# Performance work log

Hardware: AMD Instinct MI355X
Metric: run time of the kernel (lower is better)

## Reference

```python
import jax, jax.numpy as jnp
import numpy as np

D_MODEL = 64
HEADS = 8
LEVELS = 5
POINTS = 4
DH = D_MODEL // HEADS
EPS = 1e-5


def _layernorm(x, g, b):
    m = x.mean(-1, keepdims=True)
    v = ((x - m) ** 2).mean(-1, keepdims=True)
    return (x - m) / jnp.sqrt(v + EPS) * g + b


def _bilinear_sample(v, lx, ly, Hl, Wl):
    # v: (B, heads, Hl, Wl, dh); lx, ly: (B, Nq, heads, P) normalized in ~[0,1]
    # matches F.grid_sample(align_corners=False, padding_mode='zeros')
    x = lx * Wl - 0.5
    y = ly * Hl - 0.5
    x0 = jnp.floor(x)
    y0 = jnp.floor(y)
    wx = x - x0
    wy = y - y0
    x0i = x0.astype(jnp.int32)
    y0i = y0.astype(jnp.int32)
    B, heads = v.shape[0], v.shape[1]
    bidx = jnp.arange(B)[:, None, None, None]
    hidx = jnp.arange(heads)[None, None, :, None]

    def gather(yi, xi):
        valid = (xi >= 0) & (xi < Wl) & (yi >= 0) & (yi < Hl)
        xc = jnp.clip(xi, 0, Wl - 1)
        yc = jnp.clip(yi, 0, Hl - 1)
        g = v[bidx, hidx, yc, xc]  # (B, Nq, heads, P, dh)
        return g * valid[..., None].astype(v.dtype)

    return (gather(y0i, x0i) * ((1 - wx) * (1 - wy))[..., None]
            + gather(y0i, x0i + 1) * (wx * (1 - wy))[..., None]
            + gather(y0i + 1, x0i) * ((1 - wx) * wy)[..., None]
            + gather(y0i + 1, x0i + 1) * (wx * wy)[..., None])


def setup_inputs() -> dict:
    key = jax.random.key(0)
    ks = jax.random.split(key, 24)
    B, NQ = 2, 20000
    ss = np.array([[184, 184], [92, 92], [46, 46], [23, 23], [12, 12]], dtype=np.int64)
    areas = ss[:, 0] * ss[:, 1]
    lsi = np.concatenate([[0], np.cumsum(areas)[:-1]]).astype(np.int64)
    LIN = int(areas.sum())  # 45109
    s = 0.02
    inp = {
        'q_feat': jax.random.normal(ks[0], (B, NQ, D_MODEL), jnp.float32),
        'dense_voxel_flatten': jax.random.normal(ks[1], (B, LIN, D_MODEL), jnp.float32),
        'reference_points': jax.random.uniform(ks[2], (B, NQ, 2), jnp.float32),
        'q_pos': jax.random.normal(ks[3], (B, NQ, D_MODEL), jnp.float32),
        'spatial_shapes': ss,
        'level_start_index': lsi,
        'Wv': jax.random.normal(ks[4], (D_MODEL, D_MODEL), jnp.float32) * s,
        'bv': jnp.zeros((D_MODEL,), jnp.float32),
        'Wo': jax.random.normal(ks[5], (D_MODEL, HEADS * LEVELS * POINTS * 2), jnp.float32) * s,
        'bo': jax.random.normal(ks[6], (HEADS * LEVELS * POINTS * 2,), jnp.float32),
        'Wa': jax.random.normal(ks[7], (D_MODEL, HEADS * LEVELS * POINTS), jnp.float32) * s,
        'ba': jnp.zeros((HEADS * LEVELS * POINTS,), jnp.float32),
        'Wout': jax.random.normal(ks[8], (D_MODEL, D_MODEL), jnp.float32) * s,
        'bout': jnp.zeros((D_MODEL,), jnp.float32),
        'g1': jnp.ones((D_MODEL,), jnp.float32),
        'b1': jnp.zeros((D_MODEL,), jnp.float32),
        'W1': jax.random.normal(ks[9], (D_MODEL, 1024), jnp.float32) * s,
        'bff1': jnp.zeros((1024,), jnp.float32),
        'W2': jax.random.normal(ks[10], (1024, D_MODEL), jnp.float32) * s,
        'bff2': jnp.zeros((D_MODEL,), jnp.float32),
        'g2': jnp.ones((D_MODEL,), jnp.float32),
        'b2': jnp.zeros((D_MODEL,), jnp.float32),
    }
    return inp


def reference(q_feat, dense_voxel_flatten, reference_points, q_pos,
              spatial_shapes, level_start_index,
              Wv, bv, Wo, bo, Wa, ba, Wout, bout,
              g1, b1, W1, bff1, W2, bff2, g2, b2):
    B, NQ, _ = q_feat.shape
    q = q_feat + q_pos  # with_pos_embed
    value = (dense_voxel_flatten @ Wv + bv).reshape(B, -1, HEADS, DH)
    off = (q @ Wo + bo).reshape(B, NQ, HEADS, LEVELS, POINTS, 2)
    aw = jax.nn.softmax((q @ Wa + ba).reshape(B, NQ, HEADS, LEVELS * POINTS), axis=-1)
    aw = aw.reshape(B, NQ, HEADS, LEVELS, POINTS)
    # offset normalizer is (W, H) per level
    ssn = np.asarray(spatial_shapes)
    normalizer = jnp.asarray(ssn[:, ::-1].copy(), q.dtype)  # (L, 2)
    loc = reference_points[:, :, None, None, None, :] + off / normalizer[None, None, None, :, None, :]
    out = jnp.zeros((B, NQ, HEADS, DH), q.dtype)
    for l in range(LEVELS):
        Hl, Wl = int(ssn[l, 0]), int(ssn[l, 1])
        st = int(np.asarray(level_start_index)[l])
        vl = value[:, st:st + Hl * Wl].reshape(B, Hl, Wl, HEADS, DH).transpose(0, 3, 1, 2, 4)
        sampled = _bilinear_sample(vl, loc[:, :, :, l, :, 0], loc[:, :, :, l, :, 1], Hl, Wl)
        out = out + jnp.einsum('bnhpd,bnhp->bnhd', sampled, aw[:, :, :, l])
    attn_out = out.reshape(B, NQ, D_MODEL) @ Wout + bout
    x = _layernorm(q_feat + attn_out, g1, b1)  # residual + norm1 (dropout=0)
    ffn = jax.nn.relu(x @ W1 + bff1) @ W2 + bff2
    return _layernorm(x + ffn, g2, b2)
```

## Files before the change

kernel.cpp:

```cpp
#include <hip/hip_runtime.h>
#include <hip/hip_bf16.h>

#define NB 2
#define NQ 20000
#define DM 64
#define NH 8
#define NL 5
#define NP 4
#define LIN 45109
#define FFN 1024

typedef __attribute__((ext_vector_type(8))) short short8;
typedef __attribute__((ext_vector_type(4))) float f32x4;

__device__ __forceinline__ float b2f(const __hip_bfloat16 h) { return __bfloat162float(h); }
__device__ __forceinline__ float lo16f(unsigned u) { return __uint_as_float(u << 16); }
__device__ __forceinline__ float hi16f(unsigned u) { return __uint_as_float(u & 0xffff0000u); }
__device__ __forceinline__ unsigned f2bf_bits(float x) {
    unsigned u = __float_as_uint(x);
    return (u + 0x7FFFu + ((u >> 16) & 1u)) >> 16;
}

__global__ void __launch_bounds__(256)
val_proj_kernel(const float* __restrict__ dvf,
                const float* __restrict__ Wv,
                const float* __restrict__ bv,
                __hip_bfloat16* __restrict__ valA,
                __hip_bfloat16* __restrict__ valB,
                int rows) {
    __shared__ __align__(16) __hip_bfloat16 wvp[8][64][8];
    __shared__ __align__(16) __hip_bfloat16 ar[64][72];
    __shared__ __align__(16) float bvs[64];

    const int tid = threadIdx.x;
    const int lane = tid & 63;
    const int w = tid >> 6;
    const int m16 = lane & 15, qd = lane >> 4;
    const int row0 = blockIdx.x * 64;

    for (int idx = tid; idx < 4096; idx += 256) {
        const int j = idx & 7;
        const int l = (idx >> 3) & 63;
        const int seg = idx >> 9;
        const int nt = seg >> 1, kc = seg & 1;
        const int n = nt * 16 + (l & 15);
        const int k = kc * 32 + (l >> 4) * 8 + j;
        wvp[seg][l][j] = __float2bfloat16(Wv[k * 64 + n]);
    }
    if (tid < 64) bvs[tid] = bv[tid];

    {
        const int r = w * 16 + m16;
        const int grow = row0 + r;
        const int c0 = qd * 16;
        __hip_bfloat16* dst = &ar[r][c0];
        if (grow < rows) {
            const float4* src = (const float4*)&dvf[(size_t)grow * DM + c0];
#pragma unroll
            for (int t = 0; t < 4; t++) {
                const float4 v = src[t];
                dst[t * 4 + 0] = __float2bfloat16(v.x);
                dst[t * 4 + 1] = __float2bfloat16(v.y);
                dst[t * 4 + 2] = __float2bfloat16(v.z);
                dst[t * 4 + 3] = __float2bfloat16(v.w);
            }
        } else {
#pragma unroll
            for (int t = 0; t < 16; t++) dst[t] = __float2bfloat16(0.f);
        }
    }
    __syncthreads();

    f32x4 acc[4];
#pragma unroll
    for (int nt = 0; nt < 4; nt++) acc[nt] = (f32x4){0.f, 0.f, 0.f, 0.f};
#pragma unroll
    for (int kc = 0; kc < 2; kc++) {
        const short8 a = *(const short8*)&ar[w * 16 + m16][kc * 32 + qd * 8];
#pragma unroll
        for (int nt = 0; nt < 4; nt++) {
            const short8 b = *(const short8*)&wvp[nt * 2 + kc][lane][0];
            acc[nt] = __builtin_amdgcn_mfma_f32_16x16x32_bf16(a, b, acc[nt], 0, 0, 0);
        }
    }

#pragma unroll
    for (int r = 0; r < 4; r++) {
        const int gr = row0 + w * 16 + qd * 4 + r;
        if (gr < rows) {
            const int vr = (gr < LIN) ? gr : gr - LIN;
            __hip_bfloat16* dst = (gr < LIN) ? valA : valB;
#pragma unroll
            for (int nt = 0; nt < 4; nt++) {
                const int c = nt * 16 + m16;
                dst[((size_t)(c >> 3) * LIN + vr) * 8 + (c & 7)] =
                    __float2bfloat16(acc[nt][r] + bvs[c]);
            }
        }
    }
}

__global__ void pack_kernel(const float* __restrict__ W1, const float* __restrict__ W2,
                            const float* __restrict__ Wo, const float* __restrict__ Wa,
                            const float* __restrict__ Wout,
                            __hip_bfloat16* __restrict__ W1p, __hip_bfloat16* __restrict__ W2p,
                            __hip_bfloat16* __restrict__ Woap, __hip_bfloat16* __restrict__ Woutp) {
    const int t = blockIdx.x * 256 + threadIdx.x;
    const int lane = t & 63;
    const int m = lane & 15, qd = lane >> 4;
    const int seg = t >> 6;
    if (seg < 128) {
        const int nt = seg >> 1, kc = seg & 1;
        const int n = nt * 16 + m, kb = kc * 32 + qd * 8;
        __hip_bfloat16* dst = W1p + ((size_t)seg * 64 + lane) * 8;
#pragma unroll
        for (int j = 0; j < 8; j++) dst[j] = __float2bfloat16(W1[(size_t)(kb + j) * FFN + n]);
    } else if (seg < 256) {
        const int sl = seg - 128;
        const int nt = sl >> 5, kc = sl & 31;
        const int n = nt * 16 + m, kb = kc * 32 + qd * 8;
        __hip_bfloat16* dst = W2p + ((size_t)sl * 64 + lane) * 8;
#pragma unroll
        for (int j = 0; j < 8; j++) dst[j] = __float2bfloat16(W2[(size_t)(kb + j) * DM + n]);
    } else if (seg < 316) {
        const int sl = seg - 256;
        const int nt = sl >> 1, kc = sl & 1;
        const int n = nt * 16 + m, kb = kc * 32 + qd * 8;
        __hip_bfloat16* dst = Woap + ((size_t)sl * 64 + lane) * 8;
#pragma unroll
        for (int j = 0; j < 8; j++) {
            const int k = kb + j;
            const float v = (n < 320) ? Wo[(size_t)k * 320 + n] : Wa[(size_t)k * 160 + (n - 320)];
            dst[j] = __float2bfloat16(v);
        }
    } else if (seg < 324) {
        const int sl = seg - 316;
        const int nt = sl >> 1, kc = sl & 1;
        const int n = nt * 16 + m, kb = kc * 32 + qd * 8;
        __hip_bfloat16* dst = Woutp + ((size_t)sl * 64 + lane) * 8;
#pragma unroll
        for (int j = 0; j < 8; j++) dst[j] = __float2bfloat16(Wout[(size_t)(kb + j) * DM + n]);
    }
}

__global__ void __launch_bounds__(256, 8)
attn4_kernel(const float* __restrict__ q_feat,
             const float* __restrict__ ref_pts,
             const float* __restrict__ q_pos,
             const __hip_bfloat16* __restrict__ Woap,
             const float* __restrict__ bo, const float* __restrict__ ba,
             const __hip_bfloat16* __restrict__ Woutp, const float* __restrict__ bout,
             const float* __restrict__ g1, const float* __restrict__ b1,
             const __hip_bfloat16* __restrict__ valA,
             const __hip_bfloat16* __restrict__ valB,
             int qoff,
             float* __restrict__ xout) {
    __shared__ __align__(16) __hip_bfloat16 qb[16][72];
    __shared__ __align__(16) float offs[4][321];
    __shared__ __align__(16) float aws[4][161];
    __shared__ __align__(16) float refs[4][2];
    __shared__ __align__(16) int4  dsc[640];

    float (*xs4)[64] = (float(*)[64])offs;

    const int tid = threadIdx.x;
    const int lane = tid & 63;
    const int w = tid >> 6;
    const int m16 = lane & 15, qd = lane >> 4;
    const int q0 = qoff + blockIdx.x * 4;
    const int qi = q0 + w;

    const int sz[NL]  = {184, 92, 46, 23, 12};
    const int lsi[NL] = {0, 33856, 42320, 44436, 44965};

    const __hip_bfloat16* valp = (q0 >= NQ) ? valB : valA;

    const float qf = q_feat[(size_t)qi * DM + lane];
    const float qp = q_pos[(size_t)qi * DM + lane];
    qb[w][lane] = __float2bfloat16(qf + qp);
    for (int idx = tid; idx < 12 * 64; idx += 256)
        qb[4 + (idx >> 6)][idx & 63] = __float2bfloat16(0.f);
    if (tid < 8) refs[tid >> 1][tid & 1] = ref_pts[(size_t)(q0 + (tid >> 1)) * 2 + (tid & 1)];
    __syncthreads();

    for (int nt = w; nt < 30; nt += 4) {
        f32x4 acc = {0.f, 0.f, 0.f, 0.f};
#pragma unroll
        for (int kc = 0; kc < 2; kc++) {
            const short8 a = *(const short8*)&qb[m16][kc * 32 + qd * 8];
            const short8 b = *(const short8*)(Woap + ((size_t)(nt * 2 + kc) * 64 + lane) * 8);
            acc = __builtin_amdgcn_mfma_f32_16x16x32_bf16(a, b, acc, 0, 0, 0);
        }
        if (qd == 0) {
            const int n = nt * 16 + m16;
            if (n < 320) {
                const float bn = bo[n];
#pragma unroll
                for (int r = 0; r < 4; r++) offs[r][n] = acc[r] + bn;
            } else {
                const float bn = ba[n - 320];
#pragma unroll
                for (int r = 0; r < 4; r++) aws[r][n - 320] = acc[r] + bn;
            }
        }
    }
    __syncthreads();

    {
        const int g = tid >> 3;
        const int q = g >> 3, h = g & 7;
        const int j = tid & 7;
        float* p = &aws[q][h * 20];
        const float v0 = p[j], v1 = p[j + 8];
        const float v2 = (j < 4) ? p[j + 16] : -1e30f;
        float mx = fmaxf(fmaxf(v0, v1), v2);
        mx = fmaxf(mx, __shfl_xor(mx, 1, 8));
        mx = fmaxf(mx, __shfl_xor(mx, 2, 8));
        mx = fmaxf(mx, __shfl_xor(mx, 4, 8));
        const float e0 = __expf(v0 - mx), e1 = __expf(v1 - mx);
        const float e2 = (j < 4) ? __expf(v2 - mx) : 0.f;
        float s = e0 + e1 + e2;
        s += __shfl_xor(s, 1, 8);
        s += __shfl_xor(s, 2, 8);
        s += __shfl_xor(s, 4, 8);
        const float inv = 1.f / s;
        p[j] = e0 * inv;
        p[j + 8] = e1 * inv;
        if (j < 4) p[j + 16] = e2 * inv;
    }
    __syncthreads();

    for (int s = tid; s < 640; s += 256) {
        const int h = s & 7;
        const int t2 = s >> 3;
        const int p = t2 & 3;
        const int t3 = t2 >> 2;
        const int l = t3 % 5;
        const int q = t3 / 5;
        const int Wl = sz[l];
        const float Wf = (float)Wl;
        const int st = lsi[l];
        const int c = ((h * 5 + l) * 4 + p) * 2;
        const float fx = fmaf(refs[q][0], Wf, offs[q][c]) - 0.5f;
        const float fy = fmaf(refs[q][1], Wf, offs[q][c + 1]) - 0.5f;
        const float x0f = floorf(fx), y0f = floorf(fy);
        const float wx = fx - x0f, wy = fy - y0f;
        const int x0 = (int)x0f, y0 = (int)y0f;
        const float aV = aws[q][h * 20 + l * 4 + p];
        const bool xin0 = (x0 >= 0) & (x0 < Wl);
        const bool xin1 = (x0 >= -1) & (x0 < Wl - 1);
        const bool yin0 = (y0 >= 0) & (y0 < Wl);
        const bool yin1 = (y0 >= -1) & (y0 < Wl - 1);
        const float w00 = (xin0 & yin0) ? (1.f - wx) * (1.f - wy) * aV : 0.f;
        const float w10 = (xin1 & yin0) ? wx * (1.f - wy) * aV : 0.f;
        const float w01 = (xin0 & yin1) ? (1.f - wx) * wy * aV : 0.f;
        const float w11 = (xin1 & yin1) ? wx * wy * aV : 0.f;
        int b0 = (st + y0 * Wl + x0) * 8;
        b0 = b0 < -1520 ? -1520 : b0;
        b0 = b0 > LIN * 8 ? LIN * 8 : b0;
        const int b1 = b0 + Wl * 8;
        int4 d4;
        d4.x = b0;
        d4.y = b1;
        d4.z = (int)(f2bf_bits(w00) | (f2bf_bits(w10) << 16));
        d4.w = (int)(f2bf_bits(w01) | (f2bf_bits(w11) << 16));
        dsc[s] = d4;
    }
    __syncthreads();

    {
        const int h = lane >> 3, j = lane & 7;
        const int c = j & 3;
        const int sp = j >> 2;
        const __hip_bfloat16* vbase = valp + (size_t)h * (LIN * 8);
        float acc[8] = {0.f, 0.f, 0.f, 0.f, 0.f, 0.f, 0.f, 0.f};
#pragma unroll
        for (int k = 0; k < 10; k++) {
            const int s = 2 * k + sp;
            const int4 d4 = dsc[(w * 20 + s) * 8 + h];
            const int base = (c >= 2) ? d4.y : d4.x;
            const unsigned wb = (unsigned)((c >= 2) ? d4.w : d4.z);
            const float wt = (c & 1) ? hi16f(wb) : lo16f(wb);
            const short8 v = *(const short8*)(vbase + base + (c & 1) * 8);
#pragma unroll
            for (int d = 0; d < 8; d++)
                acc[d] = fmaf(wt, __uint_as_float(((unsigned)(unsigned short)v[d]) << 16), acc[d]);
        }
#pragma unroll
        for (int o = 1; o <= 4; o <<= 1)
#pragma unroll
            for (int d = 0; d < 8; d++)
                acc[d] += __shfl_xor(acc[d], o, 64);
        float r = acc[0];
#pragma unroll
        for (int d = 1; d < 8; d++) r = (j == d) ? acc[d] : r;
        qb[w][lane] = __float2bfloat16(r);
    }
    __syncthreads();

    {
        f32x4 acc = {0.f, 0.f, 0.f, 0.f};
#pragma unroll
        for (int kc = 0; kc < 2; kc++) {
            const short8 a = *(const short8*)&qb[m16][kc * 32 + qd * 8];
            const short8 b = *(const short8*)(Woutp + ((size_t)(w * 2 + kc) * 64 + lane) * 8);
            acc = __builtin_amdgcn_mfma_f32_16x16x32_bf16(a, b, acc, 0, 0, 0);
        }
        if (qd == 0) {
            const int n = w * 16 + m16;
            const float bn = bout[n];
#pragma unroll
            for (int r = 0; r < 4; r++) xs4[r][n] = acc[r] + bn;
        }
    }
    __syncthreads();

    {
        const float xpre = qf + xs4[w][lane];
        float s = xpre, s2 = xpre * xpre;
#pragma unroll
        for (int o = 32; o >= 1; o >>= 1) {
            s += __shfl_xor(s, o, 64);
            s2 += __shfl_xor(s2, o, 64);
        }
        const float mean = s * (1.f / 64.f);
        const float var = s2 * (1.f / 64.f) - mean * mean;
        const float xn = (xpre - mean) * rsqrtf(var + 1e-5f);
        xout[(size_t)qi * DM + lane] = xn * g1[lane] + b1[lane];
    }
}

__global__ void __launch_bounds__(256)
ffn_kernel(const __hip_bfloat16* __restrict__ W1p, const float* __restrict__ bff1,
           const __hip_bfloat16* __restrict__ W2p, const float* __restrict__ bff2,
           const float* __restrict__ g2, const float* __restrict__ b2,
           float* __restrict__ io) {
    __shared__ __align__(16) __hip_bfloat16 xb[32][72];
    __shared__ __align__(16) __hip_bfloat16 hb[32][264];
    __shared__ __align__(16) float yr[32][64];

    const int tid = threadIdx.x;
    const int lane = tid & 63;
    const int w = tid >> 6;
    const int m16 = lane & 15, qd = lane >> 4;
    const int q0 = blockIdx.x * 32;

    {
        const int q = tid >> 3, i = tid & 7;
        const float4 v0 = *(const float4*)&io[(size_t)(q0 + q) * DM + i * 8];
        const float4 v1 = *(const float4*)&io[(size_t)(q0 + q) * DM + i * 8 + 4];
        __hip_bfloat16* xp = &xb[q][i * 8];
        xp[0] = __float2bfloat16(v0.x); xp[1] = __float2bfloat16(v0.y);
        xp[2] = __float2bfloat16(v0.z); xp[3] = __float2bfloat16(v0.w);
        xp[4] = __float2bfloat16(v1.x); xp[5] = __float2bfloat16(v1.y);
        xp[6] = __float2bfloat16(v1.z); xp[7] = __float2bfloat16(v1.w);
    }
    __syncthreads();

    f32x4 yacc[2];
    yacc[0] = (f32x4){0.f, 0.f, 0.f, 0.f};
    yacc[1] = (f32x4){0.f, 0.f, 0.f, 0.f};

#pragma unroll
    for (int qtr = 0; qtr < 4; qtr++) {
#pragma unroll
        for (int ti = 0; ti < 4; ti++) {
            const int nt = qtr * 16 + w + ti * 4;
            f32x4 acc[2];
            acc[0] = (f32x4){0.f, 0.f, 0.f, 0.f};
            acc[1] = (f32x4){0.f, 0.f, 0.f, 0.f};
#pragma unroll
            for (int kc = 0; kc < 2; kc++) {
                const short8 b = *(const short8*)(W1p + ((size_t)(nt * 2 + kc) * 64 + lane) * 8);
#pragma unroll
                for (int mt = 0; mt < 2; mt++) {
                    const short8 a = *(const short8*)&xb[mt * 16 + m16][kc * 32 + qd * 8];
                    acc[mt] = __builtin_amdgcn_mfma_f32_16x16x32_bf16(a, b, acc[mt], 0, 0, 0);
                }
            }
            const int ncol = (nt - qtr * 16) * 16 + m16;
            const float bn = bff1[nt * 16 + m16];
#pragma unroll
            for (int mt = 0; mt < 2; mt++)
#pragma unroll
                for (int r = 0; r < 4; r++)
                    hb[mt * 16 + qd * 4 + r][ncol] = __float2bfloat16(fmaxf(acc[mt][r] + bn, 0.f));
        }
        __syncthreads();
#pragma unroll
        for (int kc2 = 0; kc2 < 8; kc2++) {
            const short8 b = *(const short8*)(W2p + ((size_t)(w * 32 + qtr * 8 + kc2) * 64 + lane) * 8);
#pragma unroll
            for (int mt = 0; mt < 2; mt++) {
                const short8 a = *(const short8*)&hb[mt * 16 + m16][kc2 * 32 + qd * 8];
                yacc[mt] = __builtin_amdgcn_mfma_f32_16x16x32_bf16(a, b, yacc[mt], 0, 0, 0);
            }
        }
        __syncthreads();
    }

    {
        const int n = w * 16 + m16;
        const float bn = bff2[n];
#pragma unroll
        for (int mt = 0; mt < 2; mt++)
#pragma unroll
            for (int r = 0; r < 4; r++) {
                const int mm = mt * 16 + qd * 4 + r;
                yr[mm][n] = yacc[mt][r] + bn;
            }
    }
    __syncthreads();

    {
        const int q = tid >> 3, i = tid & 7;
        const float4 x0 = *(const float4*)&io[(size_t)(q0 + q) * DM + i * 8];
        const float4 x1 = *(const float4*)&io[(size_t)(q0 + q) * DM + i * 8 + 4];
        float4 v0 = *(const float4*)&yr[q][i * 8];
        float4 v1 = *(const float4*)&yr[q][i * 8 + 4];
        v0.x += x0.x; v0.y += x0.y; v0.z += x0.z; v0.w += x0.w;
        v1.x += x1.x; v1.y += x1.y; v1.z += x1.z; v1.w += x1.w;
        float s = v0.x + v0.y + v0.z + v0.w + v1.x + v1.y + v1.z + v1.w;
        float s2 = v0.x * v0.x + v0.y * v0.y + v0.z * v0.z + v0.w * v0.w
                 + v1.x * v1.x + v1.y * v1.y + v1.z * v1.z + v1.w * v1.w;
#pragma unroll
        for (int o = 4; o >= 1; o >>= 1) { s += __shfl_xor(s, o, 64); s2 += __shfl_xor(s2, o, 64); }
        const float mean = s * (1.f / 64.f);
        const float var = s2 * (1.f / 64.f) - mean * mean;
        const float rstd = rsqrtf(var + 1e-5f);
        const float4 ga = *(const float4*)&g2[i * 8];
        const float4 gb = *(const float4*)&g2[i * 8 + 4];
        const float4 ba4 = *(const float4*)&b2[i * 8];
        const float4 bb4 = *(const float4*)&b2[i * 8 + 4];
        float4 o0, o1;
        o0.x = (v0.x - mean) * rstd * ga.x + ba4.x;
        o0.y = (v0.y - mean) * rstd * ga.y + ba4.y;
        o0.z = (v0.z - mean) * rstd * ga.z + ba4.z;
        o0.w = (v0.w - mean) * rstd * ga.w + ba4.w;
        o1.x = (v1.x - mean) * rstd * gb.x + bb4.x;
        o1.y = (v1.y - mean) * rstd * gb.y + bb4.y;
        o1.z = (v1.z - mean) * rstd * gb.z + bb4.z;
        o1.w = (v1.w - mean) * rstd * gb.w + bb4.w;
        *(float4*)&io[(size_t)(q0 + q) * DM + i * 8] = o0;
        *(float4*)&io[(size_t)(q0 + q) * DM + i * 8 + 4] = o1;
    }
}

extern "C" void kernel_launch(void* const* d_in, const int* in_sizes, int n_in,
                              void* d_out, int out_size, void* d_ws, size_t ws_size,
                              hipStream_t stream) {
    const int B0 = (in_sizes[4] >= 4096) ? 4 : 6;
    const float* q_feat = (const float*)d_in[0];
    const float* dvf    = (const float*)d_in[1];
    const float* refp   = (const float*)d_in[2];
    const float* q_pos  = (const float*)d_in[3];
    const float* Wv   = (const float*)d_in[B0 + 0];
    const float* bv   = (const float*)d_in[B0 + 1];
    const float* Wo   = (const float*)d_in[B0 + 2];
    const float* bo   = (const float*)d_in[B0 + 3];
    const float* Wa   = (const float*)d_in[B0 + 4];
    const float* ba   = (const float*)d_in[B0 + 5];
    const float* Wout = (const float*)d_in[B0 + 6];
    const float* bout = (const float*)d_in[B0 + 7];
    const float* g1   = (const float*)d_in[B0 + 8];
    const float* b1   = (const float*)d_in[B0 + 9];
    const float* W1   = (const float*)d_in[B0 + 10];
    const float* bff1 = (const float*)d_in[B0 + 11];
    const float* W2   = (const float*)d_in[B0 + 12];
    const float* bff2 = (const float*)d_in[B0 + 13];
    const float* g2   = (const float*)d_in[B0 + 14];
    const float* b2   = (const float*)d_in[B0 + 15];
    float* out = (float*)d_out;

    const size_t val_elems = (size_t)LIN * DM;
    const size_t pack_elems = (size_t)(128 + 128 + 60 + 8) * 64 * 8;
    const size_t PAD_ELEMS = 12288;
    const bool dbuf = ws_size >= (pack_elems + 2 * val_elems + PAD_ELEMS) * sizeof(__hip_bfloat16);

    __hip_bfloat16* W1p = (__hip_bfloat16*)d_ws;
    __hip_bfloat16* W2p = W1p + (size_t)128 * 64 * 8;
    __hip_bfloat16* Woap = W2p + (size_t)128 * 64 * 8;
    __hip_bfloat16* Woutp = Woap + (size_t)60 * 64 * 8;
    __hip_bfloat16* val0 = W1p + pack_elems;
    __hip_bfloat16* val1 = dbuf ? val0 + val_elems : val0;

    __hip_bfloat16* pad_ptr = val1 + val_elems;
    hipMemsetAsync(pad_ptr, 0, PAD_ELEMS * sizeof(__hip_bfloat16), stream);

    pack_kernel<<<81, 256, 0, stream>>>(W1, W2, Wo, Wa, Wout, W1p, W2p, Woap, Woutp);

    if (dbuf) {
        val_proj_kernel<<<(2 * LIN + 63) / 64, 256, 0, stream>>>(
            dvf, Wv, bv, val0, val1, 2 * LIN);
        attn4_kernel<<<(NB * NQ) / 4, 256, 0, stream>>>(
            q_feat, refp, q_pos, Woap, bo, ba, Woutp, bout, g1, b1,
            val0, val1, 0, out);
    } else {
        for (int b = 0; b < NB; b++) {
            val_proj_kernel<<<(LIN + 63) / 64, 256, 0, stream>>>(
                dvf + (size_t)b * val_elems, Wv, bv, val0, val0, LIN);
            attn4_kernel<<<NQ / 4, 256, 0, stream>>>(
                q_feat, refp, q_pos, Woap, bo, ba, Woutp, bout, g1, b1,
                val0, val0, b * NQ, out);
        }
    }
    ffn_kernel<<<(NB * NQ) / 32, 256, 0, stream>>>(W1p, bff1, W2p, bff2, g2, b2, out);
}
```

Baseline: 236.4 us.

## Transpose MFMA operands so outputs store as packed contiguous bf16 vectors

The value projection and FFN first GEMM swap the A and B MFMA operands, so each lane's four accumulator values land in consecutive output columns. That lets bias add and bf16 conversion be written as packed 64-bit stores instead of scalar strided stores. The sampling reduction replaces the full 8-value butterfly with a recursive halving exchange that uses fewer shuffles. The FFN input is staged in an MFMA-friendly LDS layout loaded once into registers, and zero-fill uses vector stores. This adds operand-layout complexity, and the hand-rolled f2bf conversion could differ slightly from the intrinsic.

```diff
diff --git a/kernel.cpp b/kernel.cpp
--- a/kernel.cpp
+++ b/kernel.cpp
@@ -73,28 +73,32 @@
 
     f32x4 acc[4];
 #pragma unroll
-    for (int nt = 0; nt < 4; nt++) acc[nt] = (f32x4){0.f, 0.f, 0.f, 0.f};
+    for (int mt = 0; mt < 4; mt++) acc[mt] = (f32x4){0.f, 0.f, 0.f, 0.f};
 #pragma unroll
     for (int kc = 0; kc < 2; kc++) {
-        const short8 a = *(const short8*)&ar[w * 16 + m16][kc * 32 + qd * 8];
-#pragma unroll
-        for (int nt = 0; nt < 4; nt++) {
-            const short8 b = *(const short8*)&wvp[nt * 2 + kc][lane][0];
-            acc[nt] = __builtin_amdgcn_mfma_f32_16x16x32_bf16(a, b, acc[nt], 0, 0, 0);
-        }
-    }
-
-#pragma unroll
-    for (int r = 0; r < 4; r++) {
-        const int gr = row0 + w * 16 + qd * 4 + r;
-        if (gr < rows) {
-            const int vr = (gr < LIN) ? gr : gr - LIN;
-            __hip_bfloat16* dst = (gr < LIN) ? valA : valB;
-#pragma unroll
-            for (int nt = 0; nt < 4; nt++) {
-                const int c = nt * 16 + m16;
-                dst[((size_t)(c >> 3) * LIN + vr) * 8 + (c & 7)] =
-                    __float2bfloat16(acc[nt][r] + bvs[c]);
+        const short8 b = *(const short8*)&ar[w * 16 + m16][kc * 32 + qd * 8];
+#pragma unroll
+        for (int mt = 0; mt < 4; mt++) {
+            const short8 a = *(const short8*)&wvp[mt * 2 + kc][lane][0];
+            acc[mt] = __builtin_amdgcn_mfma_f32_16x16x32_bf16(a, b, acc[mt], 0, 0, 0);
+        }
+    }
+
+    {
+        const int vg = row0 + w * 16 + m16;
+        if (vg < rows) {
+            const int vr = (vg < LIN) ? vg : vg - LIN;
+            __hip_bfloat16* dst = (vg < LIN) ? valA : valB;
+#pragma unroll
+            for (int mt = 0; mt < 4; mt++) {
+                const int c0 = mt * 16 + qd * 4;
+                const float4 bv4 = *(const float4*)&bvs[c0];
+                const float r0 = acc[mt][0] + bv4.x, r1 = acc[mt][1] + bv4.y;
+                const float r2 = acc[mt][2] + bv4.z, r3 = acc[mt][3] + bv4.w;
+                uint2 u;
+                u.x = f2bf_bits(r0) | (f2bf_bits(r1) << 16);
+                u.y = f2bf_bits(r2) | (f2bf_bits(r3) << 16);
+                *(uint2*)&dst[((size_t)(c0 >> 3) * LIN + vr) * 8 + (c0 & 7)] = u;
             }
         }
     }
@@ -178,8 +182,8 @@
     const float qf = q_feat[(size_t)qi * DM + lane];
     const float qp = q_pos[(size_t)qi * DM + lane];
     qb[w][lane] = __float2bfloat16(qf + qp);
-    for (int idx = tid; idx < 12 * 64; idx += 256)
-        qb[4 + (idx >> 6)][idx & 63] = __float2bfloat16(0.f);
+    for (int idx = tid; idx < 12 * 16; idx += 256)
+        *(uint2*)&qb[4 + (idx >> 4)][(idx & 15) * 4] = (uint2){0u, 0u};
     if (tid < 8) refs[tid >> 1][tid & 1] = ref_pts[(size_t)(q0 + (tid >> 1)) * 2 + (tid & 1)];
     __syncthreads();
 
@@ -258,10 +262,10 @@
         int b0 = (st + y0 * Wl + x0) * 8;
         b0 = b0 < -1520 ? -1520 : b0;
         b0 = b0 > LIN * 8 ? LIN * 8 : b0;
-        const int b1 = b0 + Wl * 8;
+        const int b1i = b0 + Wl * 8;
         int4 d4;
         d4.x = b0;
-        d4.y = b1;
+        d4.y = b1i;
         d4.z = (int)(f2bf_bits(w00) | (f2bf_bits(w10) << 16));
         d4.w = (int)(f2bf_bits(w01) | (f2bf_bits(w11) << 16));
         dsc[s] = d4;
@@ -286,15 +290,29 @@
             for (int d = 0; d < 8; d++)
                 acc[d] = fmaf(wt, __uint_as_float(((unsigned)(unsigned short)v[d]) << 16), acc[d]);
         }
-#pragma unroll
-        for (int o = 1; o <= 4; o <<= 1)
-#pragma unroll
-            for (int d = 0; d < 8; d++)
-                acc[d] += __shfl_xor(acc[d], o, 64);
-        float r = acc[0];
-#pragma unroll
-        for (int d = 1; d < 8; d++) r = (j == d) ? acc[d] : r;
-        qb[w][lane] = __float2bfloat16(r);
+        const bool hi4 = (j & 4) != 0;
+        float k4[4], gv4[4];
+#pragma unroll
+        for (int d = 0; d < 4; d++) {
+            k4[d] = hi4 ? acc[d + 4] : acc[d];
+            gv4[d] = hi4 ? acc[d] : acc[d + 4];
+        }
+#pragma unroll
+        for (int d = 0; d < 4; d++) k4[d] += __shfl_xor(gv4[d], 4, 64);
+        const bool hi2 = (j & 2) != 0;
+        float k2[2], gv2[2];
+#pragma unroll
+        for (int d = 0; d < 2; d++) {
+            k2[d] = hi2 ? k4[d + 2] : k4[d];
+            gv2[d] = hi2 ? k4[d] : k4[d + 2];
+        }
+#pragma unroll
+        for (int d = 0; d < 2; d++) k2[d] += __shfl_xor(gv2[d], 2, 64);
+        const bool hi1 = (j & 1) != 0;
+        float k1 = hi1 ? k2[1] : k2[0];
+        float gv1 = hi1 ? k2[0] : k2[1];
+        k1 += __shfl_xor(gv1, 1, 64);
+        qb[w][lane] = __float2bfloat16(k1);
     }
     __syncthreads();
 
@@ -335,7 +353,7 @@
            const __hip_bfloat16* __restrict__ W2p, const float* __restrict__ bff2,
            const float* __restrict__ g2, const float* __restrict__ b2,
            float* __restrict__ io) {
-    __shared__ __align__(16) __hip_bfloat16 xb[32][72];
+    __shared__ __align__(16) __hip_bfloat16 xq[2][2][64][8];
     __shared__ __align__(16) __hip_bfloat16 hb[32][264];
     __shared__ __align__(16) float yr[32][64];
 
@@ -349,13 +367,22 @@
         const int q = tid >> 3, i = tid & 7;
         const float4 v0 = *(const float4*)&io[(size_t)(q0 + q) * DM + i * 8];
         const float4 v1 = *(const float4*)&io[(size_t)(q0 + q) * DM + i * 8 + 4];
-        __hip_bfloat16* xp = &xb[q][i * 8];
-        xp[0] = __float2bfloat16(v0.x); xp[1] = __float2bfloat16(v0.y);
-        xp[2] = __float2bfloat16(v0.z); xp[3] = __float2bfloat16(v0.w);
-        xp[4] = __float2bfloat16(v1.x); xp[5] = __float2bfloat16(v1.y);
-        xp[6] = __float2bfloat16(v1.z); xp[7] = __float2bfloat16(v1.w);
-    }
-    __syncthreads();
+        uint2 ua, ub;
+        ua.x = f2bf_bits(v0.x) | (f2bf_bits(v0.y) << 16);
+        ua.y = f2bf_bits(v0.z) | (f2bf_bits(v0.w) << 16);
+        ub.x = f2bf_bits(v1.x) | (f2bf_bits(v1.y) << 16);
+        ub.y = f2bf_bits(v1.z) | (f2bf_bits(v1.w) << 16);
+        uint4 u4 = {ua.x, ua.y, ub.x, ub.y};
+        *(uint4*)&xq[q >> 4][i >> 2][(q & 15) + (i & 3) * 16][0] = u4;
+    }
+    __syncthreads();
+
+    short8 bx[2][2];
+#pragma unroll
+    for (int nt = 0; nt < 2; nt++)
+#pragma unroll
+        for (int kc = 0; kc < 2; kc++)
+            bx[nt][kc] = *(const short8*)&xq[nt][kc][lane][0];
 
     f32x4 yacc[2];
     yacc[0] = (f32x4){0.f, 0.f, 0.f, 0.f};
@@ -364,27 +391,31 @@
 #pragma unroll
     for (int qtr = 0; qtr < 4; qtr++) {
 #pragma unroll
-        for (int ti = 0; ti < 4; ti++) {
-            const int nt = qtr * 16 + w + ti * 4;
+        for (int mt = 0; mt < 4; mt++) {
+            const int htl = mt * 4 + w;
+            const int ht = qtr * 16 + htl;
             f32x4 acc[2];
             acc[0] = (f32x4){0.f, 0.f, 0.f, 0.f};
             acc[1] = (f32x4){0.f, 0.f, 0.f, 0.f};
 #pragma unroll
             for (int kc = 0; kc < 2; kc++) {
-                const short8 b = *(const short8*)(W1p + ((size_t)(nt * 2 + kc) * 64 + lane) * 8);
-#pragma unroll
-                for (int mt = 0; mt < 2; mt++) {
-                    const short8 a = *(const short8*)&xb[mt * 16 + m16][kc * 32 + qd * 8];
-                    acc[mt] = __builtin_amdgcn_mfma_f32_16x16x32_bf16(a, b, acc[mt], 0, 0, 0);
-                }
-            }
-            const int ncol = (nt - qtr * 16) * 16 + m16;
-            const float bn = bff1[nt * 16 + m16];
-#pragma unroll
-            for (int mt = 0; mt < 2; mt++)
-#pragma unroll
-                for (int r = 0; r < 4; r++)
-                    hb[mt * 16 + qd * 4 + r][ncol] = __float2bfloat16(fmaxf(acc[mt][r] + bn, 0.f));
+                const short8 a = *(const short8*)(W1p + ((size_t)(ht * 2 + kc) * 64 + lane) * 8);
+#pragma unroll
+                for (int nt = 0; nt < 2; nt++)
+                    acc[nt] = __builtin_amdgcn_mfma_f32_16x16x32_bf16(a, bx[nt][kc], acc[nt], 0, 0, 0);
+            }
+            const float4 b4 = *(const float4*)&bff1[ht * 16 + qd * 4];
+#pragma unroll
+            for (int nt = 0; nt < 2; nt++) {
+                const float r0 = fmaxf(acc[nt][0] + b4.x, 0.f);
+                const float r1 = fmaxf(acc[nt][1] + b4.y, 0.f);
+                const float r2 = fmaxf(acc[nt][2] + b4.z, 0.f);
+                const float r3 = fmaxf(acc[nt][3] + b4.w, 0.f);
+                uint2 u;
+                u.x = f2bf_bits(r0) | (f2bf_bits(r1) << 16);
+                u.y = f2bf_bits(r2) | (f2bf_bits(r3) << 16);
+                *(uint2*)&hb[nt * 16 + m16][htl * 16 + qd * 4] = u;
+            }
         }
         __syncthreads();
 #pragma unroll
```

Measured after the change: 234.0 us. No clear change (-1.0%).
